# Kernel optimization log

Measured on AMD Instinct MI355X. Metric: run time of the kernel, lower is better.

Reference implementation:

```python
import jax, jax.numpy as jnp
import numpy as np


def setup_inputs() -> dict:
    key = jax.random.key(0)
    k1, k2 = jax.random.split(key)
    B, T, F = 8, 1000, 257
    m = jax.random.normal(k1, (B, 27, T, F), dtype=jnp.float32)
    x = jax.random.normal(k2, (B, F, T, 2), dtype=jnp.float32)
    v = jnp.array([[1.0, -0.5, -0.5], [0.0, np.sqrt(3) / 2, -np.sqrt(3) / 2]], dtype=jnp.float32)
    return {"m": m, "x": x, "v": v}


def reference(m, x, v):
    B, C, T, F = m.shape
    # m -> (B, 3, 9, T, F); contract the complex-basis dim (3) with v rows
    m5 = m.reshape(B, 3, C // 3, T, F)
    H_real = jnp.einsum('k,bkntf->bntf', v[0], m5)  # (B, 9, T, F)
    H_imag = jnp.einsum('k,bkntf->bntf', v[1], m5)
    M_real = H_real.reshape(B, 3, 3, T, F)
    M_imag = H_imag.reshape(B, 3, 3, T, F)

    # x: (B,F,T,2) -> (B,2,T,F), pad: time causal (top=2), freq symmetric (1,1)
    xp = jnp.transpose(x, (0, 3, 2, 1))
    xp = jnp.pad(xp, ((0, 0), (0, 0), (2, 0), (1, 1)))
    # 3x3 unfold as 9 shifted views: (B, 2, 3, 3, T, F)
    xu = jnp.stack(
        [xp[:, :, i:i + T, j:j + F] for i in range(3) for j in range(3)],
        axis=2,
    ).reshape(B, 2, 3, 3, T, F)

    xr, xi = xu[:, 0], xu[:, 1]
    x_enh_real = jnp.sum(M_real * xr - M_imag * xi, axis=(1, 2))  # (B, T, F)
    x_enh_imag = jnp.sum(M_real * xi + M_imag * xr, axis=(1, 2))
    x_enh = jnp.stack([x_enh_real, x_enh_imag], axis=3)  # (B, T, F, 2)
    return jnp.transpose(x_enh, (0, 2, 1, 3))  # (B, F, T, 2)
```

## Files before the change

kernel.cpp:

```cpp
#include <hip/hip_runtime.h>


constexpr int B = 8, C = 27, T = 1000, F = 257;
constexpr int TCH = 4;
constexpr int NT  = T / TCH;
constexpr int BLK = 320;
constexpr int TROW  = TCH + 2;
constexpr int ROWSU = 259;
constexpr int RP    = 7;
constexpr int PLANE = 260 * RP;

__global__ __launch_bounds__(BLK, 4)
void ccm_kernel(const float* __restrict__ m,
                const float* __restrict__ x,
                float* __restrict__ out) {
    __shared__ float xs[2 * PLANE];

    const int bid = blockIdx.x;
    const int tc  = bid % NT;
    const int b   = bid / NT;
    const int t0  = tc * TCH;
    const int tx  = threadIdx.x;

    const float* xb = x + (size_t)b * F * T * 2;

    for (int p = tx; p < ROWSU * TROW; p += BLK) {
        const int row = p / TROW;
        const int tt  = p - row * TROW;
        const int f   = row - 1;
        const int t   = t0 - 2 + tt;
        float re = 0.f, im = 0.f;
        if (f >= 0 && f < F && t >= 0) {
            const float2 v = *reinterpret_cast<const float2*>(
                xb + ((size_t)f * T + t) * 2);
            re = v.x; im = v.y;
        }
        xs[row * RP + tt]         = re;
        xs[PLANE + row * RP + tt] = im;
    }
    __syncthreads();

    if (tx >= F) return;
    const int f = tx;

    const float SQ3_2 = 0.8660254037844386f;
    constexpr size_t CS = (size_t)T * F;
    const float* mb = m + ((size_t)b * C * T + t0) * F;

    float wr[3][3], wi[3][3];
    #pragma unroll
    for (int p = 0; p < 2; ++p) {
        #pragma unroll
        for (int j = 0; j < 3; ++j) {
            wr[p][j] = xs[(f + j) * RP + p];
            wi[p][j] = xs[PLANE + (f + j) * RP + p];
        }
    }

    float2 res[TCH];

#define LOADM(DST, U)                                                     \
    {                                                                     \
        _Pragma("unroll")                                                 \
        for (int n = 0; n < 27; ++n)                                      \
            DST[n] = mb[(size_t)n * CS + (size_t)(U) * F + f];            \
    }

#define STEP(AV, U)                                                       \
    {                                                                     \
        _Pragma("unroll")                                                 \
        for (int j = 0; j < 3; ++j) {                                     \
            wr[2][j] = xs[(f + j) * RP + ((U) + 2)];                      \
            wi[2][j] = xs[PLANE + (f + j) * RP + ((U) + 2)];              \
        }                                                                 \
        float accr = 0.f, acci = 0.f;                                     \
        _Pragma("unroll")                                                 \
        for (int i = 0; i < 3; ++i) {                                     \
            _Pragma("unroll")                                             \
            for (int j = 0; j < 3; ++j) {                                 \
                const int n = i * 3 + j;                                  \
                const float hr = AV[n] - 0.5f * (AV[n + 9] + AV[n + 18]); \
                const float hi = SQ3_2 * (AV[n + 9] - AV[n + 18]);        \
                accr += hr * wr[i][j] - hi * wi[i][j];                    \
                acci += hr * wi[i][j] + hi * wr[i][j];                    \
            }                                                             \
        }                                                                 \
        res[U] = make_float2(accr, acci);                                 \
        _Pragma("unroll")                                                 \
        for (int j = 0; j < 3; ++j) {                                     \
            wr[0][j] = wr[1][j]; wi[0][j] = wi[1][j];                     \
            wr[1][j] = wr[2][j]; wi[1][j] = wi[2][j];                     \
        }                                                                 \
    }

    float Am[27], Bm[27];
    LOADM(Am, 0);
    LOADM(Bm, 1);  STEP(Am, 0);
    LOADM(Am, 2);  STEP(Bm, 1);
    LOADM(Bm, 3);  STEP(Am, 2);
                   STEP(Bm, 3);

#undef LOADM
#undef STEP

    float* op = out + ((size_t)(b * F + f) * T + t0) * 2;
    #pragma unroll
    for (int u = 0; u < TCH / 2; ++u) {
        reinterpret_cast<float4*>(op)[u] =
            make_float4(res[2 * u].x, res[2 * u].y,
                        res[2 * u + 1].x, res[2 * u + 1].y);
    }
}

extern "C" void kernel_launch(void* const* d_in, const int* in_sizes, int n_in,
                              void* d_out, int out_size, void* d_ws, size_t ws_size,
                              hipStream_t stream) {
    const float* m = (const float*)d_in[0];
    const float* x = (const float*)d_in[1];
    float* out = (float*)d_out;

    const int grid = B * NT;
    ccm_kernel<<<grid, BLK, 0, stream>>>(m, x, out);
}
```

Measured before the change: 59.26 us.

## Split complex-basis channel groups across three thread groups with shared-memory reduction

Each block now has three 320-thread groups, and each group loads and processes only the 9 mask channels for one of the three complex-basis components. The v coefficient is folded into the x window instead of being applied to the mask values. Partial results from groups 1 and 2 are reduced through shared memory by group 0, which writes the output. The first mask loads are also issued before the x-tile barrier so they overlap the x staging. The intent is more memory-level parallelism and fewer registers per thread, which should raise occupancy on this bandwidth-bound kernel. The cost is an extra barrier, extra shared memory and a larger block of 960 threads.

```diff
diff --git a/kernel.cpp b/kernel.cpp
--- a/kernel.cpp
+++ b/kernel.cpp
@@ -4,65 +4,61 @@
 constexpr int B = 8, C = 27, T = 1000, F = 257;
 constexpr int TCH = 4;
 constexpr int NT  = T / TCH;
-constexpr int BLK = 320;
+constexpr int GRP = 320;
+constexpr int BLK = 3 * GRP;
 constexpr int TROW  = TCH + 2;
 constexpr int ROWSU = 259;
 constexpr int RP    = 7;
 constexpr int PLANE = 260 * RP;
+constexpr int RPITCH = 260;
 
-__global__ __launch_bounds__(BLK, 4)
+__global__ __launch_bounds__(BLK, 8)
 void ccm_kernel(const float* __restrict__ m,
                 const float* __restrict__ x,
                 float* __restrict__ out) {
     __shared__ float xs[2 * PLANE];
+    __shared__ float rs[2 * TCH * RPITCH * 2];
 
     const int bid = blockIdx.x;
     const int tc  = bid % NT;
     const int b   = bid / NT;
     const int t0  = tc * TCH;
     const int tx  = threadIdx.x;
+    const int g   = tx / GRP;
+    const int f   = tx - g * GRP;
+    const bool active = (f < F);
 
     const float* xb = x + (size_t)b * F * T * 2;
 
     for (int p = tx; p < ROWSU * TROW; p += BLK) {
         const int row = p / TROW;
         const int tt  = p - row * TROW;
-        const int f   = row - 1;
+        const int ff  = row - 1;
         const int t   = t0 - 2 + tt;
         float re = 0.f, im = 0.f;
-        if (f >= 0 && f < F && t >= 0) {
+        if (ff >= 0 && ff < F && t >= 0) {
             const float2 v = *reinterpret_cast<const float2*>(
-                xb + ((size_t)f * T + t) * 2);
+                xb + ((size_t)ff * T + t) * 2);
             re = v.x; im = v.y;
         }
         xs[row * RP + tt]         = re;
         xs[PLANE + row * RP + tt] = im;
     }
-    __syncthreads();
-
-    if (tx >= F) return;
-    const int f = tx;
 
     const float SQ3_2 = 0.8660254037844386f;
+    const float ckr = (g == 0) ? 1.0f : -0.5f;
+    const float cki = (g == 0) ? 0.0f : ((g == 1) ? SQ3_2 : -SQ3_2);
+
     constexpr size_t CS = (size_t)T * F;
-    const float* mb = m + ((size_t)b * C * T + t0) * F;
-
-    float wr[3][3], wi[3][3];
-    #pragma unroll
-    for (int p = 0; p < 2; ++p) {
-        #pragma unroll
-        for (int j = 0; j < 3; ++j) {
-            wr[p][j] = xs[(f + j) * RP + p];
-            wi[p][j] = xs[PLANE + (f + j) * RP + p];
-        }
-    }
+    const float* mb = m + (((size_t)b * C + 9 * g) * T + t0) * F;
 
     float2 res[TCH];
+    float Am[9], Bm[9];
 
 #define LOADM(DST, U)                                                     \
     {                                                                     \
         _Pragma("unroll")                                                 \
-        for (int n = 0; n < 27; ++n)                                      \
+        for (int n = 0; n < 9; ++n)                                       \
             DST[n] = mb[(size_t)n * CS + (size_t)(U) * F + f];            \
     }
 
@@ -70,8 +66,10 @@
     {                                                                     \
         _Pragma("unroll")                                                 \
         for (int j = 0; j < 3; ++j) {                                     \
-            wr[2][j] = xs[(f + j) * RP + ((U) + 2)];                      \
-            wi[2][j] = xs[PLANE + (f + j) * RP + ((U) + 2)];              \
+            const float xr = xs[(f + j) * RP + ((U) + 2)];                \
+            const float xi = xs[PLANE + (f + j) * RP + ((U) + 2)];        \
+            wr[2][j] = ckr * xr - cki * xi;                               \
+            wi[2][j] = ckr * xi + cki * xr;                               \
         }                                                                 \
         float accr = 0.f, acci = 0.f;                                     \
         _Pragma("unroll")                                                 \
@@ -79,10 +77,8 @@
             _Pragma("unroll")                                             \
             for (int j = 0; j < 3; ++j) {                                 \
                 const int n = i * 3 + j;                                  \
-                const float hr = AV[n] - 0.5f * (AV[n + 9] + AV[n + 18]); \
-                const float hi = SQ3_2 * (AV[n + 9] - AV[n + 18]);        \
-                accr += hr * wr[i][j] - hi * wi[i][j];                    \
-                acci += hr * wi[i][j] + hi * wr[i][j];                    \
+                accr += AV[n] * wr[i][j];                                 \
+                acci += AV[n] * wi[i][j];                                 \
             }                                                             \
         }                                                                 \
         res[U] = make_float2(accr, acci);                                 \
@@ -93,22 +89,60 @@
         }                                                                 \
     }
 
-    float Am[27], Bm[27];
-    LOADM(Am, 0);
-    LOADM(Bm, 1);  STEP(Am, 0);
-    LOADM(Am, 2);  STEP(Bm, 1);
-    LOADM(Bm, 3);  STEP(Am, 2);
-                   STEP(Bm, 3);
+    if (active) {
+        LOADM(Am, 0);
+        LOADM(Bm, 1);
+    }
+    __syncthreads();
 
+    float wr[3][3], wi[3][3];
+    if (active) {
+        #pragma unroll
+        for (int p = 0; p < 2; ++p) {
+            #pragma unroll
+            for (int j = 0; j < 3; ++j) {
+                const float xr = xs[(f + j) * RP + p];
+                const float xi = xs[PLANE + (f + j) * RP + p];
+                wr[p][j] = ckr * xr - cki * xi;
+                wi[p][j] = ckr * xi + cki * xr;
+            }
+        }
+
+        STEP(Am, 0);  LOADM(Am, 2);
+        STEP(Bm, 1);  LOADM(Bm, 3);
+        STEP(Am, 2);
+        STEP(Bm, 3);
+
+        if (g > 0) {
+            float2* slab = reinterpret_cast<float2*>(rs) +
+                           (size_t)(g - 1) * TCH * RPITCH;
+            #pragma unroll
+            for (int r = 0; r < TCH; ++r)
+                slab[r * RPITCH + f] = res[r];
+        }
+    }
 #undef LOADM
 #undef STEP
 
-    float* op = out + ((size_t)(b * F + f) * T + t0) * 2;
-    #pragma unroll
-    for (int u = 0; u < TCH / 2; ++u) {
-        reinterpret_cast<float4*>(op)[u] =
-            make_float4(res[2 * u].x, res[2 * u].y,
-                        res[2 * u + 1].x, res[2 * u + 1].y);
+    __syncthreads();
+
+    if (g == 0 && active) {
+        const float2* s1 = reinterpret_cast<const float2*>(rs);
+        const float2* s2 = s1 + (size_t)TCH * RPITCH;
+        #pragma unroll
+        for (int r = 0; r < TCH; ++r) {
+            const float2 p1 = s1[r * RPITCH + f];
+            const float2 p2 = s2[r * RPITCH + f];
+            res[r].x += p1.x + p2.x;
+            res[r].y += p1.y + p2.y;
+        }
+        float* op = out + ((size_t)(b * F + f) * T + t0) * 2;
+        #pragma unroll
+        for (int u = 0; u < TCH / 2; ++u) {
+            reinterpret_cast<float4*>(op)[u] =
+                make_float4(res[2 * u].x, res[2 * u].y,
+                            res[2 * u + 1].x, res[2 * u + 1].y);
+        }
     }
 }
 
```

Measured after the change: 56.57 us. -4.5%, faster.
